# Kernel optimization log

Hardware: AMD Instinct MI355X
Metric: run time of the kernel (lower is better)

## Reference

```python
import jax, jax.numpy as jnp
import numpy as np

N_NODES = 50000
N_EDGES = 800000
IN_DIM = 512
OUT_DIM = 512


def setup_inputs() -> dict:
    key = jax.random.key(0)
    ks = jax.random.split(key, 8)
    x = jax.random.normal(ks[0], (N_NODES, IN_DIM), dtype=jnp.float32)
    edge_index = jax.random.randint(ks[1], (2, N_EDGES), 0, N_NODES, dtype=jnp.int64)
    s = 1.0 / np.sqrt(IN_DIM)
    # SAGEConv params: lin_l (applied to aggregated neighbors, with bias),
    # lin_r (applied to root/self features, no bias). Two convs: loc and scale.
    Wl1 = jax.random.uniform(ks[2], (OUT_DIM, IN_DIM), jnp.float32, -s, s)
    bl1 = jnp.zeros((OUT_DIM,), jnp.float32)
    Wr1 = jax.random.uniform(ks[3], (OUT_DIM, IN_DIM), jnp.float32, -s, s)
    Wl2 = jax.random.uniform(ks[4], (OUT_DIM, IN_DIM), jnp.float32, -s, s)
    bl2 = jnp.zeros((OUT_DIM,), jnp.float32)
    Wr2 = jax.random.uniform(ks[5], (OUT_DIM, IN_DIM), jnp.float32, -s, s)
    return {"x": x, "edge_index": edge_index,
            "Wl1": Wl1, "bl1": bl1, "Wr1": Wr1,
            "Wl2": Wl2, "bl2": bl2, "Wr2": Wr2}


def _sage_conv(x, agg, Wl, bl, Wr):
    # lin_l(sum-aggregated neighbors) + lin_r(x)
    return agg @ Wl.T + bl + x @ Wr.T


def reference(x, edge_index, Wl1, bl1, Wr1, Wl2, bl2, Wr2):
    src, dst = edge_index[0], edge_index[1]
    # sum aggregation of source features into destination nodes: [N, in_dim]
    agg = jax.ops.segment_sum(x[src], dst, num_segments=N_NODES)
    loc = _sage_conv(x, agg, Wl1, bl1, Wr1)
    loc = jnp.clip(loc, -100.0, 100.0)
    scale = jax.nn.softplus(_sage_conv(x, agg, Wl2, bl2, Wr2)) + 0.001
    scale = jnp.minimum(scale, 100.0)
    return (loc, scale)
```

## Files before the change

kernel.cpp:

```cpp
#include <hip/hip_runtime.h>
#include <stdint.h>

#define N_NODES 50000
#define N_EDGES 800000
#define IN_DIM 512
#define OUT_DIM 512
#define KDIM 1024
#define NDIM 1024

typedef __bf16 bf16x8 __attribute__((ext_vector_type(8)));
typedef float f32x4 __attribute__((ext_vector_type(4)));

__device__ __forceinline__ unsigned short f2bf(float f) {
    union { float f; unsigned u; } c; c.f = f;
    unsigned u = c.u;
    u += 0x7fffu + ((u >> 16) & 1u);
    return (unsigned short)(u >> 16);
}
__device__ __forceinline__ float bf2f(unsigned short h) {
    union { unsigned u; float f; } c; c.u = ((unsigned)h) << 16;
    return c.f;
}

__global__ void xconv_kernel(const float* __restrict__ x, unsigned short* __restrict__ xb) {
    int i = blockIdx.x * blockDim.x + threadIdx.x;
    const int n4 = N_NODES * IN_DIM / 4;
    if (i < n4) {
        float4 v = ((const float4*)x)[i];
        ushort4 o;
        o.x = f2bf(v.x); o.y = f2bf(v.y); o.z = f2bf(v.z); o.w = f2bf(v.w);
        ((ushort4*)xb)[i] = o;
    }
}

__global__ void count_kernel(const int* __restrict__ ei, int* __restrict__ counts) {
    int i = blockIdx.x * blockDim.x + threadIdx.x;
    if (i < N_EDGES) {
        int dst = ei[N_EDGES + i];
        dst = min(max(dst, 0), N_NODES - 1);
        atomicAdd(&counts[dst], 1);
    }
}

__global__ __launch_bounds__(1024) void scan_local_kernel(
    const int* __restrict__ cnt, int* __restrict__ offs,
    int* __restrict__ bsums, int n) {
    __shared__ int warp_sums[16];
    int tid = threadIdx.x;
    int lane = tid & 63;
    int w = tid >> 6;
    int i = blockIdx.x * 1024 + tid;
    int v = (i < n) ? cnt[i] : 0;
    int s = v;
    #pragma unroll
    for (int d = 1; d < 64; d <<= 1) {
        int t = __shfl_up(s, d, 64);
        if (lane >= d) s += t;
    }
    if (lane == 63) warp_sums[w] = s;
    __syncthreads();
    if (w == 0) {
        int ws = (lane < 16) ? warp_sums[lane] : 0;
        #pragma unroll
        for (int d = 1; d < 16; d <<= 1) {
            int t = __shfl_up(ws, d, 64);
            if (lane >= d) ws += t;
        }
        if (lane < 16) warp_sums[lane] = ws;
    }
    __syncthreads();
    int base = (w > 0 ? warp_sums[w - 1] : 0);
    if (i < n) offs[i] = base + s - v;
    if (tid == 1023) bsums[blockIdx.x] = base + s;
}

__global__ void scan_bsums_kernel(int* __restrict__ bsums, int nb) {
    int lane = threadIdx.x & 63;
    int v = (lane < nb) ? bsums[lane] : 0;
    int s = v;
    #pragma unroll
    for (int d = 1; d < 64; d <<= 1) {
        int t = __shfl_up(s, d, 64);
        if (lane >= d) s += t;
    }
    if (lane < nb) bsums[lane] = s - v;
}

__global__ __launch_bounds__(1024) void scan_apply_kernel(
    int* __restrict__ offs, int* __restrict__ cursor,
    const int* __restrict__ bsums, const int* __restrict__ cnt, int n) {
    int i = blockIdx.x * 1024 + threadIdx.x;
    if (i < n) {
        int o = offs[i] + bsums[blockIdx.x];
        offs[i] = o;
        cursor[i] = o;
        if (i == n - 1) offs[n] = o + cnt[i];
    }
}

__global__ void fill_kernel(const int* __restrict__ ei, int* __restrict__ cursor,
                            int* __restrict__ bucket) {
    int i = blockIdx.x * blockDim.x + threadIdx.x;
    if (i < N_EDGES) {
        int src = ei[i];
        int dst = ei[N_EDGES + i];
        src = min(max(src, 0), N_NODES - 1);
        dst = min(max(dst, 0), N_NODES - 1);
        int pos = atomicAdd(&cursor[dst], 1);
        bucket[pos] = src;
    }
}

__global__ __launch_bounds__(256) void aggregate_kernel(
    const unsigned short* __restrict__ xb, const int* __restrict__ offs,
    const int* __restrict__ bucket, unsigned short* __restrict__ aggb) {
    int n = blockIdx.x;
    int t = threadIdx.x;
    int beg = offs[n], end = offs[n + 1];
    const unsigned* xw = (const unsigned*)xb;
    float ax[8] = {}, ay[8] = {};
    int e = beg;
    for (; e + 8 <= end; e += 8) {
        int idx[8];
        unsigned v[8];
        #pragma unroll
        for (int u = 0; u < 8; ++u) idx[u] = bucket[e + u];
        #pragma unroll
        for (int u = 0; u < 8; ++u) v[u] = xw[(size_t)idx[u] * (IN_DIM / 2) + t];
        #pragma unroll
        for (int u = 0; u < 8; ++u) {
            ax[u] += bf2f((unsigned short)(v[u] & 0xffffu));
            ay[u] += bf2f((unsigned short)(v[u] >> 16));
        }
    }
    for (; e < end; ++e) {
        int s = bucket[e];
        unsigned v = xw[(size_t)s * (IN_DIM / 2) + t];
        ax[0] += bf2f((unsigned short)(v & 0xffffu));
        ay[0] += bf2f((unsigned short)(v >> 16));
    }
    float sx = ((ax[0] + ax[1]) + (ax[2] + ax[3])) + ((ax[4] + ax[5]) + (ax[6] + ax[7]));
    float sy = ((ay[0] + ay[1]) + (ay[2] + ay[3])) + ((ay[4] + ay[5]) + (ay[6] + ay[7]));
    unsigned o = (unsigned)f2bf(sx) | ((unsigned)f2bf(sy) << 16);
    ((unsigned*)aggb)[(size_t)n * (IN_DIM / 2) + t] = o;
}

__global__ void wconv_kernel(const float* __restrict__ Wl1, const float* __restrict__ Wr1,
                             const float* __restrict__ Wl2, const float* __restrict__ Wr2,
                             unsigned short* __restrict__ Wb) {
    int i = blockIdx.x * blockDim.x + threadIdx.x;
    if (i < NDIM * KDIM) {
        int n = i >> 10, k = i & 1023;
        const float* src;
        if (n < 512) src = (k < 512) ? Wl1 : Wr1;
        else         src = (k < 512) ? Wl2 : Wr2;
        int nn = n & 511, kk = k & 511;
        Wb[i] = f2bf(src[nn * 512 + kk]);
    }
}

#define BM 128
#define BN 256
#define BK 64

__device__ __forceinline__ void async_copy16(const void* g, void* lds) {
    __builtin_amdgcn_global_load_lds((const __attribute__((address_space(1))) void*)g,
                                     (__attribute__((address_space(3))) void*)lds, 16, 0, 0);
}

__global__ __launch_bounds__(256, 2) void gemm_kernel(
    const unsigned short* __restrict__ aggb,
    const unsigned short* __restrict__ xb,
    const unsigned short* __restrict__ Wb,
    const float* __restrict__ bl1, const float* __restrict__ bl2,
    float* __restrict__ out) {
    constexpr int M = N_NODES;
    __shared__ unsigned short sA[BM * BK];
    __shared__ unsigned short sB[BN * BK];

    int n0 = blockIdx.x * BN;
    int m0 = blockIdx.y * BM;
    int tid = threadIdx.x;
    int lane = tid & 63;
    int w = tid >> 6;
    int wm = (w >> 1) * 64, wn = (w & 1) * 128;

    f32x4 acc[4][8] = {};

    int fr = lane & 15, q = lane >> 4;
    int sl0 = ((q ^ (fr & 7)) << 3);
    int sl1 = (((q + 4) ^ (fr & 7)) << 3);

    for (int k0 = 0; k0 < KDIM; k0 += BK) {
        const unsigned short* Asrc;
        int ak;
        if (k0 < 512) { Asrc = aggb; ak = k0; } else { Asrc = xb; ak = k0 - 512; }
        #pragma unroll
        for (int iss = 0; iss < 4; ++iss) {
            int C = iss * 256 + tid;
            int r = C >> 3, p = C & 7;
            int gr = m0 + r; if (gr >= M) gr = M - 1;
            const unsigned short* g = Asrc + (size_t)gr * 512 + ak + ((p ^ (r & 7)) << 3);
            async_copy16(g, sA + (size_t)(iss * 256 + w * 64) * 8);
        }
        #pragma unroll
        for (int iss = 0; iss < 8; ++iss) {
            int C = iss * 256 + tid;
            int r = C >> 3, p = C & 7;
            const unsigned short* g = Wb + (size_t)(n0 + r) * KDIM + k0 + ((p ^ (r & 7)) << 3);
            async_copy16(g, sB + (size_t)(iss * 256 + w * 64) * 8);
        }
        __syncthreads();

        #pragma unroll
        for (int ksub = 0; ksub < 2; ++ksub) {
            int sl = ksub ? sl1 : sl0;
            bf16x8 af[4], bfg[8];
            #pragma unroll
            for (int i = 0; i < 4; ++i)
                af[i] = *(const bf16x8*)(sA + (wm + i * 16 + fr) * BK + sl);
            #pragma unroll
            for (int j = 0; j < 8; ++j)
                bfg[j] = *(const bf16x8*)(sB + (wn + j * 16 + fr) * BK + sl);
            #pragma unroll
            for (int i = 0; i < 4; ++i)
                #pragma unroll
                for (int j = 0; j < 8; ++j)
                    acc[i][j] = __builtin_amdgcn_mfma_f32_16x16x32_bf16(af[i], bfg[j], acc[i][j], 0, 0, 0);
        }
        __syncthreads();
    }

    bool is_scale = (n0 >= 512);
    const float* bias = is_scale ? bl2 : bl1;
    float* obase = out + (is_scale ? (size_t)N_NODES * OUT_DIM : 0);
    int ncol0 = is_scale ? (n0 - 512) : n0;
    int rq = lane >> 4;
    #pragma unroll
    for (int i = 0; i < 4; ++i) {
        #pragma unroll
        for (int j = 0; j < 8; ++j) {
            int colg = ncol0 + wn + j * 16 + fr;
            float b = bias[colg];
            #pragma unroll
            for (int r = 0; r < 4; ++r) {
                int rowg = m0 + wm + i * 16 + rq * 4 + r;
                if (rowg < M) {
                    float v = acc[i][j][r] + b;
                    float res;
                    if (is_scale) {
                        float sp = fmaxf(v, 0.f) + __logf(1.f + __expf(-fabsf(v)));
                        res = fminf(sp + 0.001f, 100.f);
                    } else {
                        res = fminf(fmaxf(v, -100.f), 100.f);
                    }
                    __builtin_nontemporal_store(res, &obase[(size_t)rowg * OUT_DIM + colg]);
                }
            }
        }
    }
}

extern "C" void kernel_launch(void* const* d_in, const int* in_sizes, int n_in,
                              void* d_out, int out_size, void* d_ws, size_t ws_size,
                              hipStream_t stream) {
    const float* x       = (const float*)d_in[0];
    const int* ei        = (const int*)d_in[1];
    const float* Wl1     = (const float*)d_in[2];
    const float* bl1     = (const float*)d_in[3];
    const float* Wr1     = (const float*)d_in[4];
    const float* Wl2     = (const float*)d_in[5];
    const float* bl2     = (const float*)d_in[6];
    const float* Wr2     = (const float*)d_in[7];
    float* out = (float*)d_out;

    char* ws = (char*)d_ws;
    size_t off = 0;
    auto alloc = [&](size_t bytes) -> void* {
        void* p = ws + off;
        off = (off + bytes + 255) & ~(size_t)255;
        return p;
    };
    unsigned short* xb    = (unsigned short*)alloc((size_t)N_NODES * IN_DIM * 2);
    unsigned short* aggb  = (unsigned short*)alloc((size_t)N_NODES * IN_DIM * 2);
    unsigned short* Wb    = (unsigned short*)alloc((size_t)NDIM * KDIM * 2);
    int* counts           = (int*)alloc((size_t)(N_NODES + 1) * 4);
    int* offs             = (int*)alloc((size_t)(N_NODES + 1) * 4);
    int* cursor           = (int*)alloc((size_t)N_NODES * 4);
    int* bucket           = (int*)alloc((size_t)N_EDGES * 4);
    int* bsums            = (int*)alloc(64 * 4);

    hipMemsetAsync(counts, 0, (size_t)(N_NODES + 1) * 4, stream);

    const int nb = (N_NODES + 1023) / 1024;

    xconv_kernel<<<(N_NODES * IN_DIM / 4 + 255) / 256, 256, 0, stream>>>(x, xb);
    count_kernel<<<(N_EDGES + 255) / 256, 256, 0, stream>>>(ei, counts);
    scan_local_kernel<<<nb, 1024, 0, stream>>>(counts, offs, bsums, N_NODES);
    scan_bsums_kernel<<<1, 64, 0, stream>>>(bsums, nb);
    scan_apply_kernel<<<nb, 1024, 0, stream>>>(offs, cursor, bsums, counts, N_NODES);
    fill_kernel<<<(N_EDGES + 255) / 256, 256, 0, stream>>>(ei, cursor, bucket);
    aggregate_kernel<<<N_NODES, 256, 0, stream>>>(xb, offs, bucket, aggb);
    wconv_kernel<<<(NDIM * KDIM + 255) / 256, 256, 0, stream>>>(Wl1, Wr1, Wl2, Wr2, Wb);

    dim3 g(NDIM / BN, (N_NODES + BM - 1) / BM);
    gemm_kernel<<<g, 256, 0, stream>>>(aggb, xb, Wb, bl1, bl2, out);
}
```

Baseline: 647.8 us.

## Use wave-per-node aggregation and smaller GEMM tiles with XCD-aware block remap

New measurement: 600.0 us. 7.4% less time.

```diff
diff --git a/kernel.cpp b/kernel.cpp
--- a/kernel.cpp
+++ b/kernel.cpp
@@ -114,35 +114,53 @@
 __global__ __launch_bounds__(256) void aggregate_kernel(
     const unsigned short* __restrict__ xb, const int* __restrict__ offs,
     const int* __restrict__ bucket, unsigned short* __restrict__ aggb) {
-    int n = blockIdx.x;
-    int t = threadIdx.x;
+    int wid = threadIdx.x >> 6;
+    int lane = threadIdx.x & 63;
+    int n = blockIdx.x * 4 + wid;
+    if (n >= N_NODES) return;
     int beg = offs[n], end = offs[n + 1];
-    const unsigned* xw = (const unsigned*)xb;
-    float ax[8] = {}, ay[8] = {};
+    float a0[8] = {}, a1[8] = {};
     int e = beg;
-    for (; e + 8 <= end; e += 8) {
-        int idx[8];
-        unsigned v[8];
-        #pragma unroll
-        for (int u = 0; u < 8; ++u) idx[u] = bucket[e + u];
-        #pragma unroll
-        for (int u = 0; u < 8; ++u) v[u] = xw[(size_t)idx[u] * (IN_DIM / 2) + t];
-        #pragma unroll
-        for (int u = 0; u < 8; ++u) {
-            ax[u] += bf2f((unsigned short)(v[u] & 0xffffu));
-            ay[u] += bf2f((unsigned short)(v[u] >> 16));
-        }
+    for (; e + 4 <= end; e += 4) {
+        int s0 = bucket[e + 0];
+        int s1 = bucket[e + 1];
+        int s2 = bucket[e + 2];
+        int s3 = bucket[e + 3];
+        uint4 v0 = *(const uint4*)(xb + (size_t)s0 * IN_DIM + lane * 8);
+        uint4 v1 = *(const uint4*)(xb + (size_t)s1 * IN_DIM + lane * 8);
+        uint4 v2 = *(const uint4*)(xb + (size_t)s2 * IN_DIM + lane * 8);
+        uint4 v3 = *(const uint4*)(xb + (size_t)s3 * IN_DIM + lane * 8);
+        a0[0] += bf2f((unsigned short)(v0.x & 0xffffu)); a0[1] += bf2f((unsigned short)(v0.x >> 16));
+        a0[2] += bf2f((unsigned short)(v0.y & 0xffffu)); a0[3] += bf2f((unsigned short)(v0.y >> 16));
+        a0[4] += bf2f((unsigned short)(v0.z & 0xffffu)); a0[5] += bf2f((unsigned short)(v0.z >> 16));
+        a0[6] += bf2f((unsigned short)(v0.w & 0xffffu)); a0[7] += bf2f((unsigned short)(v0.w >> 16));
+        a1[0] += bf2f((unsigned short)(v1.x & 0xffffu)); a1[1] += bf2f((unsigned short)(v1.x >> 16));
+        a1[2] += bf2f((unsigned short)(v1.y & 0xffffu)); a1[3] += bf2f((unsigned short)(v1.y >> 16));
+        a1[4] += bf2f((unsigned short)(v1.z & 0xffffu)); a1[5] += bf2f((unsigned short)(v1.z >> 16));
+        a1[6] += bf2f((unsigned short)(v1.w & 0xffffu)); a1[7] += bf2f((unsigned short)(v1.w >> 16));
+        a0[0] += bf2f((unsigned short)(v2.x & 0xffffu)); a0[1] += bf2f((unsigned short)(v2.x >> 16));
+        a0[2] += bf2f((unsigned short)(v2.y & 0xffffu)); a0[3] += bf2f((unsigned short)(v2.y >> 16));
+        a0[4] += bf2f((unsigned short)(v2.z & 0xffffu)); a0[5] += bf2f((unsigned short)(v2.z >> 16));
+        a0[6] += bf2f((unsigned short)(v2.w & 0xffffu)); a0[7] += bf2f((unsigned short)(v2.w >> 16));
+        a1[0] += bf2f((unsigned short)(v3.x & 0xffffu)); a1[1] += bf2f((unsigned short)(v3.x >> 16));
+        a1[2] += bf2f((unsigned short)(v3.y & 0xffffu)); a1[3] += bf2f((unsigned short)(v3.y >> 16));
+        a1[4] += bf2f((unsigned short)(v3.z & 0xffffu)); a1[5] += bf2f((unsigned short)(v3.z >> 16));
+        a1[6] += bf2f((unsigned short)(v3.w & 0xffffu)); a1[7] += bf2f((unsigned short)(v3.w >> 16));
     }
     for (; e < end; ++e) {
         int s = bucket[e];
-        unsigned v = xw[(size_t)s * (IN_DIM / 2) + t];
-        ax[0] += bf2f((unsigned short)(v & 0xffffu));
-        ay[0] += bf2f((unsigned short)(v >> 16));
-    }
-    float sx = ((ax[0] + ax[1]) + (ax[2] + ax[3])) + ((ax[4] + ax[5]) + (ax[6] + ax[7]));
-    float sy = ((ay[0] + ay[1]) + (ay[2] + ay[3])) + ((ay[4] + ay[5]) + (ay[6] + ay[7]));
-    unsigned o = (unsigned)f2bf(sx) | ((unsigned)f2bf(sy) << 16);
-    ((unsigned*)aggb)[(size_t)n * (IN_DIM / 2) + t] = o;
+        uint4 v = *(const uint4*)(xb + (size_t)s * IN_DIM + lane * 8);
+        a0[0] += bf2f((unsigned short)(v.x & 0xffffu)); a0[1] += bf2f((unsigned short)(v.x >> 16));
+        a0[2] += bf2f((unsigned short)(v.y & 0xffffu)); a0[3] += bf2f((unsigned short)(v.y >> 16));
+        a0[4] += bf2f((unsigned short)(v.z & 0xffffu)); a0[5] += bf2f((unsigned short)(v.z >> 16));
+        a0[6] += bf2f((unsigned short)(v.w & 0xffffu)); a0[7] += bf2f((unsigned short)(v.w >> 16));
+    }
+    uint4 o;
+    o.x = (unsigned)f2bf(a0[0] + a1[0]) | ((unsigned)f2bf(a0[1] + a1[1]) << 16);
+    o.y = (unsigned)f2bf(a0[2] + a1[2]) | ((unsigned)f2bf(a0[3] + a1[3]) << 16);
+    o.z = (unsigned)f2bf(a0[4] + a1[4]) | ((unsigned)f2bf(a0[5] + a1[5]) << 16);
+    o.w = (unsigned)f2bf(a0[6] + a1[6]) | ((unsigned)f2bf(a0[7] + a1[7]) << 16);
+    *(uint4*)(aggb + (size_t)n * IN_DIM + lane * 8) = o;
 }
 
 __global__ void wconv_kernel(const float* __restrict__ Wl1, const float* __restrict__ Wr1,
@@ -160,8 +178,11 @@
 }
 
 #define BM 128
-#define BN 256
+#define BN 128
 #define BK 64
+#define NT_TILES (NDIM / BN)
+#define MT_TILES ((N_NODES + BM - 1) / BM)
+#define NWG (NT_TILES * MT_TILES)
 
 __device__ __forceinline__ void async_copy16(const void* g, void* lds) {
     __builtin_amdgcn_global_load_lds((const __attribute__((address_space(1))) void*)g,
@@ -178,14 +199,19 @@
     __shared__ unsigned short sA[BM * BK];
     __shared__ unsigned short sB[BN * BK];
 
-    int n0 = blockIdx.x * BN;
-    int m0 = blockIdx.y * BM;
+    int bid = blockIdx.x;
+    int logical = (bid & 7) * (NWG / 8) + (bid >> 3);
+    int nt = logical & (NT_TILES - 1);
+    int mt = logical >> 3;
+    int n0 = nt * BN;
+    int m0 = mt * BM;
+
     int tid = threadIdx.x;
     int lane = tid & 63;
     int w = tid >> 6;
-    int wm = (w >> 1) * 64, wn = (w & 1) * 128;
-
-    f32x4 acc[4][8] = {};
+    int wm = (w >> 1) * 64, wn = (w & 1) * 64;
+
+    f32x4 acc[4][4] = {};
 
     int fr = lane & 15, q = lane >> 4;
     int sl0 = ((q ^ (fr & 7)) << 3);
@@ -204,7 +230,7 @@
             async_copy16(g, sA + (size_t)(iss * 256 + w * 64) * 8);
         }
         #pragma unroll
-        for (int iss = 0; iss < 8; ++iss) {
+        for (int iss = 0; iss < 4; ++iss) {
             int C = iss * 256 + tid;
             int r = C >> 3, p = C & 7;
             const unsigned short* g = Wb + (size_t)(n0 + r) * KDIM + k0 + ((p ^ (r & 7)) << 3);
@@ -215,17 +241,17 @@
         #pragma unroll
         for (int ksub = 0; ksub < 2; ++ksub) {
             int sl = ksub ? sl1 : sl0;
-            bf16x8 af[4], bfg[8];
+            bf16x8 af[4], bfg[4];
             #pragma unroll
             for (int i = 0; i < 4; ++i)
                 af[i] = *(const bf16x8*)(sA + (wm + i * 16 + fr) * BK + sl);
             #pragma unroll
-            for (int j = 0; j < 8; ++j)
+            for (int j = 0; j < 4; ++j)
                 bfg[j] = *(const bf16x8*)(sB + (wn + j * 16 + fr) * BK + sl);
             #pragma unroll
             for (int i = 0; i < 4; ++i)
                 #pragma unroll
-                for (int j = 0; j < 8; ++j)
+                for (int j = 0; j < 4; ++j)
                     acc[i][j] = __builtin_amdgcn_mfma_f32_16x16x32_bf16(af[i], bfg[j], acc[i][j], 0, 0, 0);
         }
         __syncthreads();
@@ -239,7 +265,7 @@
     #pragma unroll
     for (int i = 0; i < 4; ++i) {
         #pragma unroll
-        for (int j = 0; j < 8; ++j) {
+        for (int j = 0; j < 4; ++j) {
             int colg = ncol0 + wn + j * 16 + fr;
             float b = bias[colg];
             #pragma unroll
@@ -300,9 +326,8 @@
     scan_bsums_kernel<<<1, 64, 0, stream>>>(bsums, nb);
     scan_apply_kernel<<<nb, 1024, 0, stream>>>(offs, cursor, bsums, counts, N_NODES);
     fill_kernel<<<(N_EDGES + 255) / 256, 256, 0, stream>>>(ei, cursor, bucket);
-    aggregate_kernel<<<N_NODES, 256, 0, stream>>>(xb, offs, bucket, aggb);
+    aggregate_kernel<<<(N_NODES + 3) / 4, 256, 0, stream>>>(xb, offs, bucket, aggb);
     wconv_kernel<<<(NDIM * KDIM + 255) / 256, 256, 0, stream>>>(Wl1, Wr1, Wl2, Wr2, Wb);
 
-    dim3 g(NDIM / BN, (N_NODES + BM - 1) / BM);
-    gemm_kernel<<<g, 256, 0, stream>>>(aggb, xb, Wb, bl1, bl2, out);
-}
+    gemm_kernel<<<NWG, 256, 0, stream>>>(aggb, xb, Wb, bl1, bl2, out);
+}
```
